# Kernel tuning notes

Measured on AMD Instinct MI355X. Metric: run time of the kernel, lower is better.

## Reference

```python
import jax, jax.numpy as jnp
import numpy as np

BATCH, GROUPS, ARITY, OUT_DIM = 1024, 512, 4, 64


def _high_order_act(X, params):
    # X: [B, G, K]; params: [G, 2**K, D]
    A_ind = jnp.argsort(X, axis=2)                                   # [B,G,K] int
    A_sort = jnp.take_along_axis(X, A_ind, axis=2)                   # sorted values
    # barycentric-style coefficients: smallest value, then successive gaps
    coef = jnp.concatenate(
        [A_sort[:, :, :1], A_sort[:, :, 1:] - A_sort[:, :, :-1]], axis=2
    )                                                                 # [B,G,K]
    # reversed cumulative sum of 2**A_ind -> vertex index into 2**K table
    pow2 = jnp.left_shift(jnp.int32(1), A_ind.astype(jnp.int32))      # [B,G,K]
    idx = jnp.flip(jnp.cumsum(jnp.flip(pow2, axis=2), axis=2), axis=2)  # [B,G,K]
    G = params.shape[0]
    g_idx = jnp.arange(G)[None, :, None]                              # [1,G,1]
    pg = params[g_idx, idx]                                           # [B,G,K,D] gather
    return jnp.einsum('bgk,bgkd->bgd', coef, pg)                      # [B,G,D]


def setup_inputs() -> dict:
    key = jax.random.key(0)
    k1, k2 = jax.random.split(key)
    X = jax.random.normal(k1, (BATCH, GROUPS, ARITY), dtype=jnp.float32)
    params = jax.random.normal(k2, (GROUPS, 2 ** ARITY, OUT_DIM), dtype=jnp.float32)
    return {"X": X, "params": params}


def reference(X, params):
    return _high_order_act(X, params)
```

## Files before the change

kernel.cpp:

```cpp
#include <hip/hip_runtime.h>

#define BATCH   1024
#define GROUPS  512

typedef float f32x4 __attribute__((ext_vector_type(4)));

__global__ __launch_bounds__(256) void hoact_kernel(
    const float4* __restrict__ X4,
    const float4* __restrict__ P4,
    float4*       __restrict__ O4)
{
    const int tid = threadIdx.x;
    const int b   = blockIdx.x >> 1;
    const int h   = blockIdx.x & 1;
    const int w   = tid >> 6;
    const int gl  = (tid >> 4) & 3;
    const int c4  = tid & 15;

    const int  gw0  = h * 256 + w * 64;
    const long xoff = (long)b * GROUPS;
    const long ooff = (long)b * (GROUPS * 16);

#pragma unroll
    for (int half = 0; half < 2; ++half) {
        float4 xv[8];
#pragma unroll
        for (int j = 0; j < 8; ++j) {
            const int g = gw0 + (half * 8 + j) * 4 + gl;
            xv[j] = X4[xoff + g];
        }

#pragma unroll
        for (int j = 0; j < 8; ++j) {
            const int g = gw0 + (half * 8 + j) * 4 + gl;
            const float4 x = xv[j];

            float v0 = __uint_as_float((__float_as_uint(x.x) & ~3u) | 0u);
            float v1 = __uint_as_float((__float_as_uint(x.y) & ~3u) | 1u);
            float v2 = __uint_as_float((__float_as_uint(x.z) & ~3u) | 2u);
            float v3 = __uint_as_float((__float_as_uint(x.w) & ~3u) | 3u);

#define CSWAP(a, b_)                                 \
            {                                        \
                const float lo = fminf((a), (b_));   \
                const float hi = fmaxf((a), (b_));   \
                (a) = lo; (b_) = hi;                 \
            }
            CSWAP(v0, v1);
            CSWAP(v2, v3);
            CSWAP(v0, v2);
            CSWAP(v1, v3);
            CSWAP(v1, v2);
#undef CSWAP

            const int i1 = __float_as_uint(v1) & 3;
            const int i2 = __float_as_uint(v2) & 3;
            const int i3 = __float_as_uint(v3) & 3;

            const float c0 = v0;
            const float c1 = v1 - v0;
            const float c2 = v2 - v1;
            const float c3 = v3 - v2;

            const int e3 = 1 << i3;
            const int e2 = e3 + (1 << i2);
            const int e1 = e2 + (1 << i1);

            const int  gbase = g << 8;
            const f32x4 p0 = *(const f32x4*)&P4[gbase + (15 << 4) + c4];
            const f32x4 p1 = *(const f32x4*)&P4[gbase + (e1 << 4) + c4];
            const f32x4 p2 = *(const f32x4*)&P4[gbase + (e2 << 4) + c4];
            const f32x4 p3 = *(const f32x4*)&P4[gbase + (e3 << 4) + c4];

            f32x4 o;
            o.x = c0 * p0.x + c1 * p1.x + c2 * p2.x + c3 * p3.x;
            o.y = c0 * p0.y + c1 * p1.y + c2 * p2.y + c3 * p3.y;
            o.z = c0 * p0.z + c1 * p1.z + c2 * p2.z + c3 * p3.z;
            o.w = c0 * p0.w + c1 * p1.w + c2 * p2.w + c3 * p3.w;

            __builtin_nontemporal_store(o, (f32x4*)&O4[ooff + (g << 4) + c4]);
        }
    }
}

extern "C" void kernel_launch(void* const* d_in, const int* in_sizes, int n_in,
                              void* d_out, int out_size, void* d_ws, size_t ws_size,
                              hipStream_t stream) {
    const float4* X4 = (const float4*)d_in[0];
    const float4* P4 = (const float4*)d_in[1];
    float4*       O4 = (float4*)d_out;

    const int grid = BATCH * 2;
    hipLaunchKernelGGL(hoact_kernel, dim3(grid), dim3(256), 0, stream,
                       X4, P4, O4);
}
```

Measured before the change: 180.2 us.

## Stage per-group param table in LDS and remap blocks to group-major with XCD grouping

Each block now owns one group and 256 batch rows. It loads that group's 16x64 parameter table into shared memory once and gathers from LDS instead of global memory. The block index is decoded so that groups stay local to an XCD, and the second half of the X loads is prefetched while the first half is computed. The nontemporal output store is replaced by a plain store. In exchange, the output write pattern becomes strided across batch rows within a block, and LDS gathers can hit bank conflicts.

Measured after the change: 150.9 us. -16.3%, faster.

```diff
diff --git a/kernel.cpp b/kernel.cpp
--- a/kernel.cpp
+++ b/kernel.cpp
@@ -2,38 +2,48 @@
 
 #define BATCH   1024
 #define GROUPS  512
-
-typedef float f32x4 __attribute__((ext_vector_type(4)));
 
 __global__ __launch_bounds__(256) void hoact_kernel(
     const float4* __restrict__ X4,
     const float4* __restrict__ P4,
     float4*       __restrict__ O4)
 {
-    const int tid = threadIdx.x;
-    const int b   = blockIdx.x >> 1;
-    const int h   = blockIdx.x & 1;
-    const int w   = tid >> 6;
-    const int gl  = (tid >> 4) & 3;
-    const int c4  = tid & 15;
+    __shared__ float tbl[16 * 64];
 
-    const int  gw0  = h * 256 + w * 64;
-    const long xoff = (long)b * GROUPS;
-    const long ooff = (long)b * (GROUPS * 16);
+    const int xcd   = blockIdx.x & 7;
+    const int idx   = blockIdx.x >> 3;
+    const int g     = xcd * 64 + (idx & 63);
+    const int chunk = idx >> 6;
+    const int b0    = chunk * 256;
+    const int tid   = threadIdx.x;
+
+    {
+        const float4 v = P4[g * 256 + tid];
+        *(float4*)&tbl[tid << 2] = v;
+    }
+
+    const int bl = tid >> 4;
+    const int c4 = tid & 15;
+
+    float4 xv[8];
+#pragma unroll
+    for (int p = 0; p < 8; ++p)
+        xv[p] = X4[(b0 + p * 16 + bl) * GROUPS + g];
+
+    __syncthreads();
+
+    const float4 p0 = *(const float4*)&tbl[15 * 64 + (c4 << 2)];
 
 #pragma unroll
     for (int half = 0; half < 2; ++half) {
-        float4 xv[8];
 #pragma unroll
-        for (int j = 0; j < 8; ++j) {
-            const int g = gw0 + (half * 8 + j) * 4 + gl;
-            xv[j] = X4[xoff + g];
-        }
+        for (int p = 0; p < 8; ++p) {
+            const int pass = half * 8 + p;
+            const int b    = b0 + pass * 16 + bl;
+            const float4 x = xv[p];
 
-#pragma unroll
-        for (int j = 0; j < 8; ++j) {
-            const int g = gw0 + (half * 8 + j) * 4 + gl;
-            const float4 x = xv[j];
+            if (half == 0)
+                xv[p] = X4[(b0 + (8 + p) * 16 + bl) * GROUPS + g];
 
             float v0 = __uint_as_float((__float_as_uint(x.x) & ~3u) | 0u);
             float v1 = __uint_as_float((__float_as_uint(x.y) & ~3u) | 1u);
@@ -66,19 +76,17 @@
             const int e2 = e3 + (1 << i2);
             const int e1 = e2 + (1 << i1);
 
-            const int  gbase = g << 8;
-            const f32x4 p0 = *(const f32x4*)&P4[gbase + (15 << 4) + c4];
-            const f32x4 p1 = *(const f32x4*)&P4[gbase + (e1 << 4) + c4];
-            const f32x4 p2 = *(const f32x4*)&P4[gbase + (e2 << 4) + c4];
-            const f32x4 p3 = *(const f32x4*)&P4[gbase + (e3 << 4) + c4];
+            const float4 p1 = *(const float4*)&tbl[(e1 << 6) + (c4 << 2)];
+            const float4 p2 = *(const float4*)&tbl[(e2 << 6) + (c4 << 2)];
+            const float4 p3 = *(const float4*)&tbl[(e3 << 6) + (c4 << 2)];
 
-            f32x4 o;
+            float4 o;
             o.x = c0 * p0.x + c1 * p1.x + c2 * p2.x + c3 * p3.x;
             o.y = c0 * p0.y + c1 * p1.y + c2 * p2.y + c3 * p3.y;
             o.z = c0 * p0.z + c1 * p1.z + c2 * p2.z + c3 * p3.z;
             o.w = c0 * p0.w + c1 * p1.w + c2 * p2.w + c3 * p3.w;
 
-            __builtin_nontemporal_store(o, (f32x4*)&O4[ooff + (g << 4) + c4]);
+            O4[b * (GROUPS * 16) + g * 16 + c4] = o;
         }
     }
 }
@@ -90,7 +98,7 @@
     const float4* P4 = (const float4*)d_in[1];
     float4*       O4 = (float4*)d_out;
 
-    const int grid = BATCH * 2;
+    const int grid = 2048;
     hipLaunchKernelGGL(hoact_kernel, dim3(grid), dim3(256), 0, stream,
                        X4, P4, O4);
 }
```
